# Optimization experiments

Measured on AMD Instinct MI355X. Metric: run time of the kernel, lower is better.

The kernel has to match this reference:

```python
import jax, jax.numpy as jnp
import numpy as np
import math

WIDTH = 1024
DATA_WIDTH = 1024
HEADS = 16


def setup_inputs() -> dict:
    key = jax.random.key(0)
    ks = jax.random.split(key, 8)
    bs, n_ctx, n_data = 2, 1024, 4096
    init_scale = 0.25 / math.sqrt(WIDTH)
    inp = {
        "x": jax.random.normal(ks[0], (bs, n_ctx, WIDTH), dtype=jnp.float32),
        "data": jax.random.normal(ks[1], (bs, n_data, DATA_WIDTH), dtype=jnp.float32),
        "Wq": jax.random.normal(ks[2], (WIDTH, WIDTH), dtype=jnp.float32) * init_scale,
        "bq": jnp.zeros((WIDTH,), dtype=jnp.float32),
        "Wkv": jax.random.normal(ks[3], (DATA_WIDTH, 2 * WIDTH), dtype=jnp.float32) * init_scale,
        "bkv": jnp.zeros((2 * WIDTH,), dtype=jnp.float32),
        "Wproj": jax.random.normal(ks[4], (WIDTH, WIDTH), dtype=jnp.float32) * init_scale,
        "bproj": jnp.zeros((WIDTH,), dtype=jnp.float32),
    }
    return inp


def reference(x, data, Wq, bq, Wkv, bkv, Wproj, bproj):
    bs, n_ctx, _ = x.shape
    _, n_data, _ = data.shape
    h = HEADS
    attn_ch = WIDTH // h  # = (2*width)//heads//2
    scale = 1.0 / math.sqrt(math.sqrt(attn_ch))

    q = x @ Wq + bq                      # [bs, n_ctx, width]
    kv = data @ Wkv + bkv                # [bs, n_data, 2*width]

    q = q.reshape(bs, n_ctx, h, attn_ch)
    kv = kv.reshape(bs, n_data, h, 2 * attn_ch)
    k, v = kv[..., :attn_ch], kv[..., attn_ch:]

    # full O(n_ctx * n_data) attention weights, softmax in fp32 (faithful to use_flash=False path)
    weight = jnp.einsum('bthc,bshc->bhts', q * scale, k * scale)
    wdtype = weight.dtype
    weight = jax.nn.softmax(weight.astype(jnp.float32), axis=-1).astype(wdtype)
    out = jnp.einsum('bhts,bshc->bthc', weight, v).reshape(bs, n_ctx, WIDTH)

    return out @ Wproj + bproj
```

## Files before the change

kernel.cpp:

```cpp
#include <hip/hip_runtime.h>
#include <hip/hip_bf16.h>


typedef __bf16 bf16;
typedef float f32x4 __attribute__((ext_vector_type(4)));
typedef bf16 bf16x4 __attribute__((ext_vector_type(4)));
typedef bf16 bf16x8 __attribute__((ext_vector_type(8)));

#define MFMA16(A, B, C) __builtin_amdgcn_mfma_f32_16x16x32_bf16((A), (B), (C), 0, 0, 0)

constexpr int BS = 2;
constexpr int NCTX = 1024;
constexpr int NDATA = 4096;
constexpr int WID = 1024;
constexpr int NH = 16;
constexpr int DH = 64;
constexpr int NSPLIT = 4;
constexpr float ATT_SCALE = 0.35355339059327373f;

__device__ __forceinline__ void gload16(const void* g, void* l) {
  __builtin_amdgcn_global_load_lds(
      (const __attribute__((address_space(1))) unsigned int*)g,
      (__attribute__((address_space(3))) unsigned int*)l, 16, 0, 0);
}

__global__ __launch_bounds__(256) void f32_to_bf16_kernel(
    const float* __restrict__ in, bf16* __restrict__ out) {
  const size_t i = ((size_t)blockIdx.x * 256 + threadIdx.x) * 8;
  float4 v0 = *reinterpret_cast<const float4*>(&in[i]);
  float4 v1 = *reinterpret_cast<const float4*>(&in[i + 4]);
  bf16x8 o;
  o[0] = (bf16)v0.x; o[1] = (bf16)v0.y; o[2] = (bf16)v0.z; o[3] = (bf16)v0.w;
  o[4] = (bf16)v1.x; o[5] = (bf16)v1.y; o[6] = (bf16)v1.z; o[7] = (bf16)v1.w;
  *reinterpret_cast<bf16x8*>(&out[i]) = o;
}

__global__ __launch_bounds__(256) void transpose_conv_kernel(
    const float* __restrict__ in, bf16* __restrict__ outh, int R, int C) {
  __shared__ float tile[64][65];
  const int tid = threadIdx.x;
  const int c0 = blockIdx.x * 64, r0 = blockIdx.y * 64;
#pragma unroll
  for (int i = 0; i < 16; ++i) {
    int idx = tid + i * 256;
    int row = idx >> 6, col = idx & 63;
    tile[row][col] = in[(size_t)(r0 + row) * C + (c0 + col)];
  }
  __syncthreads();
#pragma unroll
  for (int i = 0; i < 16; ++i) {
    int idx = tid + i * 256;
    int orow = idx >> 6, ocol = idx & 63;
    outh[(size_t)(c0 + orow) * R + (r0 + ocol)] = (bf16)tile[ocol][orow];
  }
}

#define GEMM_MAINLOOP(Aptr, Bptr)                                              \
  __shared__ bf16 As[128][32];                                                 \
  __shared__ bf16 Bs[128][32];                                                 \
  const int tid = threadIdx.x, lane = tid & 63, w = tid >> 6;                  \
  const int wm = (w & 1) * 64, wn = (w >> 1) * 64;                             \
  const int l15 = lane & 15, l4 = lane >> 4;                                   \
  const int srow = w * 32 + (lane >> 2);                                       \
  const int scolb = (lane & 3) * 16;                                           \
  const char* a_src = (const char*)((Aptr) + (size_t)(m0 + srow) * 1024) + scolb; \
  const char* b_src = (const char*)((Bptr) + (size_t)(n0 + srow) * 1024) + scolb; \
  bf16* lds_a0 = &As[w * 32][0];                                               \
  bf16* lds_a1 = &As[w * 32 + 16][0];                                          \
  bf16* lds_b0 = &Bs[w * 32][0];                                               \
  bf16* lds_b1 = &Bs[w * 32 + 16][0];                                          \
  f32x4 acc[4][4] = {};                                                        \
  for (int kt = 0; kt < 32; ++kt) {                                            \
    __syncthreads();                                                           \
    gload16(a_src + kt * 64, lds_a0);                                          \
    gload16(a_src + kt * 64 + 16 * 2048, lds_a1);                              \
    gload16(b_src + kt * 64, lds_b0);                                          \
    gload16(b_src + kt * 64 + 16 * 2048, lds_b1);                              \
    __syncthreads();                                                           \
    bf16x8 af[4], bfr[4];                                                      \
    _Pragma("unroll") for (int mi = 0; mi < 4; ++mi)                           \
        af[mi] = *reinterpret_cast<const bf16x8*>(&As[wm + mi * 16 + l15][l4 * 8]); \
    _Pragma("unroll") for (int ni = 0; ni < 4; ++ni)                           \
        bfr[ni] = *reinterpret_cast<const bf16x8*>(&Bs[wn + ni * 16 + l15][l4 * 8]); \
    _Pragma("unroll") for (int mi = 0; mi < 4; ++mi)                           \
        _Pragma("unroll") for (int ni = 0; ni < 4; ++ni)                       \
            acc[mi][ni] = MFMA16(af[mi], bfr[ni], acc[mi][ni]);                \
  }

__global__ __launch_bounds__(256) void gemm_q_kernel(
    const bf16* __restrict__ X,
    const bf16* __restrict__ WT,
    const float* __restrict__ bias,
    bf16* __restrict__ Q) {
  const int nt = blockIdx.x & 7, mt = blockIdx.x >> 3;
  const int m0 = mt * 128, n0 = nt * 128;
  GEMM_MAINLOOP(X, WT)
#pragma unroll
  for (int ni = 0; ni < 4; ++ni) {
    int n = n0 + wn + ni * 16 + l15;
    float bv = bias[n];
    int h = n >> 6, d = n & 63;
#pragma unroll
    for (int mi = 0; mi < 4; ++mi)
#pragma unroll
      for (int r = 0; r < 4; ++r) {
        int m = m0 + wm + mi * 16 + l4 * 4 + r;
        int b = m >> 10, t = m & 1023;
        Q[(((size_t)(b * NH + h)) * NCTX + t) * DH + d] =
            (bf16)((acc[mi][ni][r] + bv) * ATT_SCALE);
      }
  }
}

__global__ __launch_bounds__(256) void gemm_kv_kernel(
    const bf16* __restrict__ DATA,
    const bf16* __restrict__ WT,
    const float* __restrict__ bias,
    bf16* __restrict__ Kb,
    bf16* __restrict__ Vt) {
  const int nt = blockIdx.x & 15, mt = blockIdx.x >> 4;
  const int m0 = mt * 128, n0 = nt * 128;
  GEMM_MAINLOOP(DATA, WT)
#pragma unroll
  for (int ni = 0; ni < 4; ++ni) {
    int n = n0 + wn + ni * 16 + l15;
    float bv = bias[n];
    int h = n >> 7, c = n & 127;
#pragma unroll
    for (int mi = 0; mi < 4; ++mi)
#pragma unroll
      for (int r = 0; r < 4; ++r) {
        int m = m0 + wm + mi * 16 + l4 * 4 + r;
        int b = m >> 12, s = m & 4095;
        float vv = acc[mi][ni][r] + bv;
        if (c < DH) {
          Kb[(((size_t)(b * NH + h)) * NDATA + s) * DH + c] = (bf16)(vv * ATT_SCALE);
        } else {
          Vt[(((size_t)(b * NH + h)) * DH + (c - DH)) * NDATA + s] = (bf16)vv;
        }
      }
  }
}

__global__ __launch_bounds__(256) void gemm_proj_kernel(
    const bf16* __restrict__ A,
    const bf16* __restrict__ WT,
    const float* __restrict__ bias,
    float* __restrict__ OUT) {
  const int nt = blockIdx.x & 7, mt = blockIdx.x >> 3;
  const int m0 = mt * 128, n0 = nt * 128;
  GEMM_MAINLOOP(A, WT)
#pragma unroll
  for (int ni = 0; ni < 4; ++ni) {
    int n = n0 + wn + ni * 16 + l15;
    float bv = bias[n];
#pragma unroll
    for (int mi = 0; mi < 4; ++mi)
#pragma unroll
      for (int r = 0; r < 4; ++r) {
        int m = m0 + wm + mi * 16 + l4 * 4 + r;
        OUT[(size_t)m * 1024 + n] = acc[mi][ni][r] + bv;
      }
  }
}

__global__ __launch_bounds__(256) void attn_kernel(
    const bf16* __restrict__ Q,
    const bf16* __restrict__ Kb,
    const bf16* __restrict__ Vt,
    bf16* __restrict__ Op,
    float* __restrict__ Ls) {
  constexpr int SCH = 32;
  constexpr int NIT = (NDATA / NSPLIT) / SCH;
  __shared__ bf16 Ks[2][SCH][72];
  __shared__ bf16 Vs[2][DH][40];
  __shared__ bf16 plds[4][16][40];
  const int tid = threadIdx.x, lane = tid & 63, w = tid >> 6;
  const int wg = (blockIdx.x & 7) * 256 + (blockIdx.x >> 3);
  const int tt = wg & 15, sp = (wg >> 4) & 3, h = (wg >> 6) & 15, b = wg >> 10;
  const int t0 = tt * 64 + w * 16;
  const int l15 = lane & 15, l4 = lane >> 4;
  const size_t qbase = (((size_t)(b * NH + h)) * NCTX + t0) * DH;
  const size_t kbase = ((size_t)(b * NH + h)) * NDATA * DH;
  const size_t vbase = ((size_t)(b * NH + h)) * DH * NDATA;

  bf16x8 qf0 = *reinterpret_cast<const bf16x8*>(&Q[qbase + (size_t)l15 * DH + l4 * 8]);
  bf16x8 qf1 = *reinterpret_cast<const bf16x8*>(&Q[qbase + (size_t)l15 * DH + 32 + l4 * 8]);

  const int krs = tid >> 3, kcs = (tid & 7) * 8;
  const int vrd = tid >> 2, vcs = (tid & 3) * 8;

  f32x4 o[4] = {};
  float lsum[4] = {0.f, 0.f, 0.f, 0.f};

  const int sstart = sp * (NDATA / NSPLIT);
  {
    bf16x8 k0 = *reinterpret_cast<const bf16x8*>(&Kb[kbase + (size_t)(sstart + krs) * DH + kcs]);
    bf16x8 v0 = *reinterpret_cast<const bf16x8*>(&Vt[vbase + (size_t)vrd * NDATA + sstart + vcs]);
    *reinterpret_cast<bf16x8*>(&Ks[0][krs][kcs]) = k0;
    *reinterpret_cast<bf16x8*>(&Vs[0][vrd][vcs]) = v0;
  }
  __syncthreads();

  int cur = 0;
  for (int it = 0; it < NIT; ++it) {
    const int s0 = sstart + it * SCH;
    bf16x8 knext, vnext;
    if (it + 1 < NIT) {
      knext = *reinterpret_cast<const bf16x8*>(&Kb[kbase + (size_t)(s0 + SCH + krs) * DH + kcs]);
      vnext = *reinterpret_cast<const bf16x8*>(&Vt[vbase + (size_t)vrd * NDATA + s0 + SCH + vcs]);
    }
#pragma unroll
    for (int sg = 0; sg < 2; ++sg) {
      bf16x8 kf0 = *reinterpret_cast<const bf16x8*>(&Ks[cur][sg * 16 + l15][l4 * 8]);
      bf16x8 kf1 = *reinterpret_cast<const bf16x8*>(&Ks[cur][sg * 16 + l15][32 + l4 * 8]);
      f32x4 ac = {};
      ac = MFMA16(qf0, kf0, ac);
      ac = MFMA16(qf1, kf1, ac);
#pragma unroll
      for (int r = 0; r < 4; ++r) {
        float e = __expf(ac[r]);
        lsum[r] += e;
        plds[w][l4 * 4 + r][sg * 16 + l15] = (bf16)e;
      }
    }
    bf16x8 pa = *reinterpret_cast<const bf16x8*>(&plds[w][l15][l4 * 8]);
#pragma unroll
    for (int dg = 0; dg < 4; ++dg) {
      bf16x8 vf = *reinterpret_cast<const bf16x8*>(&Vs[cur][dg * 16 + l15][l4 * 8]);
      o[dg] = MFMA16(pa, vf, o[dg]);
    }
    if (it + 1 < NIT) {
      *reinterpret_cast<bf16x8*>(&Ks[cur ^ 1][krs][kcs]) = knext;
      *reinterpret_cast<bf16x8*>(&Vs[cur ^ 1][vrd][vcs]) = vnext;
    }
    __syncthreads();
    cur ^= 1;
  }

  const size_t obase = (((size_t)((sp * BS + b) * NH + h)) * NCTX + t0);
#pragma unroll
  for (int r = 0; r < 4; ++r) {
    float s = lsum[r];
    s += __shfl_xor(s, 1, 64);
    s += __shfl_xor(s, 2, 64);
    s += __shfl_xor(s, 4, 64);
    s += __shfl_xor(s, 8, 64);
    if (l15 == 0) Ls[obase + l4 * 4 + r] = s;
  }
#pragma unroll
  for (int dg = 0; dg < 4; ++dg)
#pragma unroll
    for (int r = 0; r < 4; ++r)
      Op[(obase + l4 * 4 + r) * DH + dg * 16 + l15] = (bf16)o[dg][r];
}

__global__ __launch_bounds__(256) void attn_combine_kernel(
    const bf16* __restrict__ Op, const float* __restrict__ Ls,
    bf16* __restrict__ AO) {
  const int idx = blockIdx.x * 256 + threadIdx.x;
  const int d = idx & 63;
  const int t = (idx >> 6) & (NCTX - 1);
  const int h = (idx >> 16) & (NH - 1);
  const int b = idx >> 20;
  float os = 0.f, ls = 0.f;
#pragma unroll
  for (int p = 0; p < NSPLIT; ++p) {
    size_t base = ((size_t)((p * BS + b) * NH + h)) * NCTX + t;
    os += (float)Op[base * DH + d];
    ls += Ls[base];
  }
  AO[((size_t)b * NCTX + t) * WID + h * DH + d] = (bf16)(os / ls);
}

extern "C" void kernel_launch(void* const* d_in, const int* in_sizes, int n_in,
                              void* d_out, int out_size, void* d_ws, size_t ws_size,
                              hipStream_t stream) {
  const float* x = (const float*)d_in[0];
  const float* data = (const float*)d_in[1];
  const float* Wq = (const float*)d_in[2];
  const float* bq = (const float*)d_in[3];
  const float* Wkv = (const float*)d_in[4];
  const float* bkv = (const float*)d_in[5];
  const float* Wproj = (const float*)d_in[6];
  const float* bproj = (const float*)d_in[7];
  float* out = (float*)d_out;

  char* ws = (char*)d_ws;
  size_t off = 0;
  auto alloc = [&](size_t bytes) -> void* {
    void* p = ws + off;
    off += (bytes + 255) & ~(size_t)255;
    return p;
  };
  bf16* d16 = (bf16*)alloc((size_t)BS * NDATA * WID * 2);
  bf16* x16 = (bf16*)alloc((size_t)BS * NCTX * WID * 2);
  bf16* qbuf = (bf16*)alloc((size_t)BS * NH * NCTX * DH * 2);
  bf16* kbuf = (bf16*)alloc((size_t)BS * NH * NDATA * DH * 2);
  bf16* vt = (bf16*)alloc((size_t)BS * NH * DH * NDATA * 2);
  bf16* wqT = (bf16*)alloc((size_t)WID * WID * 2);
  bf16* wkvT = (bf16*)alloc((size_t)2 * WID * WID * 2);
  bf16* wprojT = (bf16*)alloc((size_t)WID * WID * 2);
  float* lsbuf = (float*)alloc((size_t)NSPLIT * BS * NH * NCTX * 4);
  bf16* opbuf = d16;
  bf16* aobuf = x16;

  f32_to_bf16_kernel<<<dim3(BS * NCTX * WID / 2048), 256, 0, stream>>>(x, x16);
  f32_to_bf16_kernel<<<dim3(BS * NDATA * WID / 2048), 256, 0, stream>>>(data, d16);

  transpose_conv_kernel<<<dim3(16, 16), 256, 0, stream>>>(Wq, wqT, WID, WID);
  transpose_conv_kernel<<<dim3(32, 16), 256, 0, stream>>>(Wkv, wkvT, WID, 2 * WID);
  transpose_conv_kernel<<<dim3(16, 16), 256, 0, stream>>>(Wproj, wprojT, WID, WID);

  gemm_q_kernel<<<dim3((BS * NCTX / 128) * (WID / 128)), 256, 0, stream>>>(x16, wqT, bq, qbuf);
  gemm_kv_kernel<<<dim3((BS * NDATA / 128) * (2 * WID / 128)), 256, 0, stream>>>(
      d16, wkvT, bkv, kbuf, vt);
  attn_kernel<<<dim3(BS * NH * (NCTX / 64) * NSPLIT), 256, 0, stream>>>(
      qbuf, kbuf, vt, opbuf, lsbuf);
  attn_combine_kernel<<<dim3(BS * NCTX * WID / 256), 256, 0, stream>>>(opbuf, lsbuf, aobuf);
  gemm_proj_kernel<<<dim3((BS * NCTX / 128) * (WID / 128)), 256, 0, stream>>>(
      aobuf, wprojT, bproj, out);
}
```

Measured before the change: 283.6 us.

## Use direct-to-LDS swizzled loads and register-resident P in attention; merge prep kernels

The attention kernel now loads K and V tiles with global_load_lds into XOR-swizzled unpadded shared buffers instead of staging through registers. It computes S transposed (K as the A operand), so the exponentiated probabilities land directly in the register layout needed for the PV MFMA, which removes the plds shared-memory round trip and collapses the row-sum to one value per lane. Separately, the two conversion launches and three weight-transpose launches are merged into one launch each to cut launch overhead. The swizzle index arithmetic is intricate and could cause correctness problems if any offset is wrong.

```diff
diff --git a/kernel.cpp b/kernel.cpp
--- a/kernel.cpp
+++ b/kernel.cpp
@@ -24,22 +24,43 @@
       (__attribute__((address_space(3))) unsigned int*)l, 16, 0, 0);
 }
 
-__global__ __launch_bounds__(256) void f32_to_bf16_kernel(
-    const float* __restrict__ in, bf16* __restrict__ out) {
-  const size_t i = ((size_t)blockIdx.x * 256 + threadIdx.x) * 8;
-  float4 v0 = *reinterpret_cast<const float4*>(&in[i]);
-  float4 v1 = *reinterpret_cast<const float4*>(&in[i + 4]);
+__global__ __launch_bounds__(256) void convert_kernel(
+    const float* __restrict__ x, const float* __restrict__ data,
+    bf16* __restrict__ x16, bf16* __restrict__ d16) {
+  const int bid = blockIdx.x;
+  const float* src;
+  bf16* dst;
+  size_t i;
+  if (bid < 1024) {
+    src = x; dst = x16; i = ((size_t)bid * 256 + threadIdx.x) * 8;
+  } else {
+    src = data; dst = d16; i = ((size_t)(bid - 1024) * 256 + threadIdx.x) * 8;
+  }
+  float4 v0 = *reinterpret_cast<const float4*>(&src[i]);
+  float4 v1 = *reinterpret_cast<const float4*>(&src[i + 4]);
   bf16x8 o;
   o[0] = (bf16)v0.x; o[1] = (bf16)v0.y; o[2] = (bf16)v0.z; o[3] = (bf16)v0.w;
   o[4] = (bf16)v1.x; o[5] = (bf16)v1.y; o[6] = (bf16)v1.z; o[7] = (bf16)v1.w;
-  *reinterpret_cast<bf16x8*>(&out[i]) = o;
-}
-
-__global__ __launch_bounds__(256) void transpose_conv_kernel(
-    const float* __restrict__ in, bf16* __restrict__ outh, int R, int C) {
+  *reinterpret_cast<bf16x8*>(&dst[i]) = o;
+}
+
+__global__ __launch_bounds__(256) void transpose_all_kernel(
+    const float* __restrict__ Wq, const float* __restrict__ Wkv,
+    const float* __restrict__ Wproj, bf16* __restrict__ wqT,
+    bf16* __restrict__ wkvT, bf16* __restrict__ wprojT) {
   __shared__ float tile[64][65];
-  const int tid = threadIdx.x;
-  const int c0 = blockIdx.x * 64, r0 = blockIdx.y * 64;
+  const int bid = blockIdx.x, tid = threadIdx.x;
+  const float* in;
+  bf16* out;
+  int R = 1024, C, cx, ry;
+  if (bid < 256) {
+    in = Wq; out = wqT; C = 1024; cx = bid & 15; ry = bid >> 4;
+  } else if (bid < 768) {
+    int t = bid - 256; in = Wkv; out = wkvT; C = 2048; cx = t & 31; ry = t >> 5;
+  } else {
+    int t = bid - 768; in = Wproj; out = wprojT; C = 1024; cx = t & 15; ry = t >> 4;
+  }
+  const int c0 = cx * 64, r0 = ry * 64;
 #pragma unroll
   for (int i = 0; i < 16; ++i) {
     int idx = tid + i * 256;
@@ -51,7 +72,7 @@
   for (int i = 0; i < 16; ++i) {
     int idx = tid + i * 256;
     int orow = idx >> 6, ocol = idx & 63;
-    outh[(size_t)(c0 + orow) * R + (r0 + ocol)] = (bf16)tile[ocol][orow];
+    out[(size_t)(c0 + orow) * R + (r0 + ocol)] = (bf16)tile[ocol][orow];
   }
 }
 
@@ -88,10 +109,8 @@
   }
 
 __global__ __launch_bounds__(256) void gemm_q_kernel(
-    const bf16* __restrict__ X,
-    const bf16* __restrict__ WT,
-    const float* __restrict__ bias,
-    bf16* __restrict__ Q) {
+    const bf16* __restrict__ X, const bf16* __restrict__ WT,
+    const float* __restrict__ bias, bf16* __restrict__ Q) {
   const int nt = blockIdx.x & 7, mt = blockIdx.x >> 3;
   const int m0 = mt * 128, n0 = nt * 128;
   GEMM_MAINLOOP(X, WT)
@@ -113,10 +132,8 @@
 }
 
 __global__ __launch_bounds__(256) void gemm_kv_kernel(
-    const bf16* __restrict__ DATA,
-    const bf16* __restrict__ WT,
-    const float* __restrict__ bias,
-    bf16* __restrict__ Kb,
+    const bf16* __restrict__ DATA, const bf16* __restrict__ WT,
+    const float* __restrict__ bias, bf16* __restrict__ Kb,
     bf16* __restrict__ Vt) {
   const int nt = blockIdx.x & 15, mt = blockIdx.x >> 4;
   const int m0 = mt * 128, n0 = nt * 128;
@@ -143,10 +160,8 @@
 }
 
 __global__ __launch_bounds__(256) void gemm_proj_kernel(
-    const bf16* __restrict__ A,
-    const bf16* __restrict__ WT,
-    const float* __restrict__ bias,
-    float* __restrict__ OUT) {
+    const bf16* __restrict__ A, const bf16* __restrict__ WT,
+    const float* __restrict__ bias, float* __restrict__ OUT) {
   const int nt = blockIdx.x & 7, mt = blockIdx.x >> 3;
   const int m0 = mt * 128, n0 = nt * 128;
   GEMM_MAINLOOP(A, WT)
@@ -172,9 +187,8 @@
     float* __restrict__ Ls) {
   constexpr int SCH = 32;
   constexpr int NIT = (NDATA / NSPLIT) / SCH;
-  __shared__ bf16 Ks[2][SCH][72];
-  __shared__ bf16 Vs[2][DH][40];
-  __shared__ bf16 plds[4][16][40];
+  __shared__ bf16 Ks[2][32][64];
+  __shared__ bf16 Vs[2][64][32];
   const int tid = threadIdx.x, lane = tid & 63, w = tid >> 6;
   const int wg = (blockIdx.x & 7) * 256 + (blockIdx.x >> 3);
   const int tt = wg & 15, sp = (wg >> 4) & 3, h = (wg >> 6) & 15, b = wg >> 10;
@@ -187,67 +201,71 @@
   bf16x8 qf0 = *reinterpret_cast<const bf16x8*>(&Q[qbase + (size_t)l15 * DH + l4 * 8]);
   bf16x8 qf1 = *reinterpret_cast<const bf16x8*>(&Q[qbase + (size_t)l15 * DH + 32 + l4 * 8]);
 
-  const int krs = tid >> 3, kcs = (tid & 7) * 8;
-  const int vrd = tid >> 2, vcs = (tid & 3) * 8;
+  const int krow0 = ((l15 >> 2) << 3) + (l15 & 3);
+  const int kf_swz = ((l15 & 3) | (((l15 >> 2) & 1) << 2)) << 4;
+  const int koff_a = ((l4 * 16) ^ kf_swz) >> 1;
+  const int koff_b = ((64 + l4 * 16) ^ kf_swz) >> 1;
+  const int voff = ((l4 * 16) ^ ((l15 & 3) << 4)) >> 1;
+
+  const int kst_off = (w * 8 + (lane >> 3)) * 128 +
+      (((lane & 7) * 16) ^ (((((lane >> 3) & 3)) | ((w & 1) << 2)) << 4));
+  const int vrow_g = w * 16 + (lane >> 2);
+  const char* vrowp = (const char*)(Vt + vbase + (size_t)vrow_g * NDATA);
+  const int vst_coff = ((lane & 3) * 16) ^ ((((lane >> 2) & 3)) << 4);
+  const char* kchunk = (const char*)(Kb + kbase);
 
   f32x4 o[4] = {};
-  float lsum[4] = {0.f, 0.f, 0.f, 0.f};
+  float lsum = 0.f;
 
   const int sstart = sp * (NDATA / NSPLIT);
-  {
-    bf16x8 k0 = *reinterpret_cast<const bf16x8*>(&Kb[kbase + (size_t)(sstart + krs) * DH + kcs]);
-    bf16x8 v0 = *reinterpret_cast<const bf16x8*>(&Vt[vbase + (size_t)vrd * NDATA + sstart + vcs]);
-    *reinterpret_cast<bf16x8*>(&Ks[0][krs][kcs]) = k0;
-    *reinterpret_cast<bf16x8*>(&Vs[0][vrd][vcs]) = v0;
-  }
+  gload16(kchunk + (size_t)sstart * 128 + kst_off, &Ks[0][w * 8][0]);
+  gload16(vrowp + (size_t)sstart * 2 + vst_coff, &Vs[0][w * 16][0]);
   __syncthreads();
 
   int cur = 0;
   for (int it = 0; it < NIT; ++it) {
     const int s0 = sstart + it * SCH;
-    bf16x8 knext, vnext;
     if (it + 1 < NIT) {
-      knext = *reinterpret_cast<const bf16x8*>(&Kb[kbase + (size_t)(s0 + SCH + krs) * DH + kcs]);
-      vnext = *reinterpret_cast<const bf16x8*>(&Vt[vbase + (size_t)vrd * NDATA + s0 + SCH + vcs]);
-    }
-#pragma unroll
-    for (int sg = 0; sg < 2; ++sg) {
-      bf16x8 kf0 = *reinterpret_cast<const bf16x8*>(&Ks[cur][sg * 16 + l15][l4 * 8]);
-      bf16x8 kf1 = *reinterpret_cast<const bf16x8*>(&Ks[cur][sg * 16 + l15][32 + l4 * 8]);
-      f32x4 ac = {};
-      ac = MFMA16(qf0, kf0, ac);
-      ac = MFMA16(qf1, kf1, ac);
-#pragma unroll
-      for (int r = 0; r < 4; ++r) {
-        float e = __expf(ac[r]);
-        lsum[r] += e;
-        plds[w][l4 * 4 + r][sg * 16 + l15] = (bf16)e;
-      }
-    }
-    bf16x8 pa = *reinterpret_cast<const bf16x8*>(&plds[w][l15][l4 * 8]);
+      gload16(kchunk + (size_t)(s0 + SCH) * 128 + kst_off, &Ks[cur ^ 1][w * 8][0]);
+      gload16(vrowp + (size_t)(s0 + SCH) * 2 + vst_coff, &Vs[cur ^ 1][w * 16][0]);
+    }
+    f32x4 p0 = {}, p1 = {};
+    {
+      bf16x8 a00 = *reinterpret_cast<const bf16x8*>(&Ks[cur][krow0][koff_a]);
+      bf16x8 a01 = *reinterpret_cast<const bf16x8*>(&Ks[cur][krow0][koff_b]);
+      p0 = MFMA16(a00, qf0, p0);
+      p0 = MFMA16(a01, qf1, p0);
+      bf16x8 a10 = *reinterpret_cast<const bf16x8*>(&Ks[cur][krow0 + 4][koff_a]);
+      bf16x8 a11 = *reinterpret_cast<const bf16x8*>(&Ks[cur][krow0 + 4][koff_b]);
+      p1 = MFMA16(a10, qf0, p1);
+      p1 = MFMA16(a11, qf1, p1);
+    }
+    bf16x8 paf;
+#pragma unroll
+    for (int r = 0; r < 4; ++r) {
+      float e = __expf(p0[r]);
+      lsum += e;
+      paf[r] = (bf16)e;
+    }
+#pragma unroll
+    for (int r = 0; r < 4; ++r) {
+      float e = __expf(p1[r]);
+      lsum += e;
+      paf[4 + r] = (bf16)e;
+    }
 #pragma unroll
     for (int dg = 0; dg < 4; ++dg) {
-      bf16x8 vf = *reinterpret_cast<const bf16x8*>(&Vs[cur][dg * 16 + l15][l4 * 8]);
-      o[dg] = MFMA16(pa, vf, o[dg]);
-    }
-    if (it + 1 < NIT) {
-      *reinterpret_cast<bf16x8*>(&Ks[cur ^ 1][krs][kcs]) = knext;
-      *reinterpret_cast<bf16x8*>(&Vs[cur ^ 1][vrd][vcs]) = vnext;
+      bf16x8 vf = *reinterpret_cast<const bf16x8*>(&Vs[cur][dg * 16 + l15][voff]);
+      o[dg] = MFMA16(paf, vf, o[dg]);
     }
     __syncthreads();
     cur ^= 1;
   }
 
   const size_t obase = (((size_t)((sp * BS + b) * NH + h)) * NCTX + t0);
-#pragma unroll
-  for (int r = 0; r < 4; ++r) {
-    float s = lsum[r];
-    s += __shfl_xor(s, 1, 64);
-    s += __shfl_xor(s, 2, 64);
-    s += __shfl_xor(s, 4, 64);
-    s += __shfl_xor(s, 8, 64);
-    if (l15 == 0) Ls[obase + l4 * 4 + r] = s;
-  }
+  lsum += __shfl_xor(lsum, 16, 64);
+  lsum += __shfl_xor(lsum, 32, 64);
+  if (l4 == 0) Ls[obase + l15] = lsum;
 #pragma unroll
   for (int dg = 0; dg < 4; ++dg)
 #pragma unroll
@@ -305,12 +323,8 @@
   bf16* opbuf = d16;
   bf16* aobuf = x16;
 
-  f32_to_bf16_kernel<<<dim3(BS * NCTX * WID / 2048), 256, 0, stream>>>(x, x16);
-  f32_to_bf16_kernel<<<dim3(BS * NDATA * WID / 2048), 256, 0, stream>>>(data, d16);
-
-  transpose_conv_kernel<<<dim3(16, 16), 256, 0, stream>>>(Wq, wqT, WID, WID);
-  transpose_conv_kernel<<<dim3(32, 16), 256, 0, stream>>>(Wkv, wkvT, WID, 2 * WID);
-  transpose_conv_kernel<<<dim3(16, 16), 256, 0, stream>>>(Wproj, wprojT, WID, WID);
+  convert_kernel<<<dim3(1024 + 4096), 256, 0, stream>>>(x, data, x16, d16);
+  transpose_all_kernel<<<dim3(1024), 256, 0, stream>>>(Wq, Wkv, Wproj, wqT, wkvT, wprojT);
 
   gemm_q_kernel<<<dim3((BS * NCTX / 128) * (WID / 128)), 256, 0, stream>>>(x16, wqT, bq, qbuf);
   gemm_kv_kernel<<<dim3((BS * NDATA / 128) * (2 * WID / 128)), 256, 0, stream>>>(
```

New measurement: 266.2 us. 1.07x faster.
